# Kernel optimization log

Measured on AMD Instinct MI355X. Metric: run time of the kernel, lower is better.

## Reference

```python
import jax, jax.numpy as jnp
import numpy as np

N = 100_000        # nodes
F_IN = 1024        # input features
H1, C1 = 8, 8      # layer-1 heads, per-head channels (concat -> 64)
C_OUT = 40         # num classes (layer-2, heads=1, concat=False)
E = 3_200_000      # directed edges (avg degree 32)
NEG_SLOPE = 0.2    # PyG GATConv default leaky_relu slope


def setup_inputs() -> dict:
    key = jax.random.key(0)
    ks = jax.random.split(key, 10)
    x = jax.random.normal(ks[0], (N, F_IN), jnp.float32)
    edge_index = jax.random.randint(ks[1], (2, E), 0, N, dtype=jnp.int32)
    s1 = 1.0 / np.sqrt(F_IN)
    W1 = jax.random.normal(ks[2], (F_IN, H1 * C1), jnp.float32) * s1
    sa = 1.0 / np.sqrt(C1)
    att_src1 = jax.random.normal(ks[3], (H1, C1), jnp.float32) * sa
    att_dst1 = jax.random.normal(ks[4], (H1, C1), jnp.float32) * sa
    b1 = jnp.zeros((H1 * C1,), jnp.float32)
    s2 = 1.0 / np.sqrt(H1 * C1)
    W2 = jax.random.normal(ks[5], (H1 * C1, C_OUT), jnp.float32) * s2
    so = 1.0 / np.sqrt(C_OUT)
    att_src2 = jax.random.normal(ks[6], (1, C_OUT), jnp.float32) * so
    att_dst2 = jax.random.normal(ks[7], (1, C_OUT), jnp.float32) * so
    b2 = jnp.zeros((C_OUT,), jnp.float32)
    return {"x": x, "edge_index": edge_index, "W1": W1, "att_src1": att_src1,
            "att_dst1": att_dst1, "b1": b1, "W2": W2, "att_src2": att_src2,
            "att_dst2": att_dst2, "b2": b2}


def gat_layer(x, src, dst, W, a_src, a_dst, b, heads, ch, concat, n):
    # per-head linear projection: [n, heads, ch]
    xw = (x @ W).reshape(n, heads, ch)
    # per-node attention logits: [n, heads]
    al_src = jnp.einsum('nhc,hc->nh', xw, a_src)
    al_dst = jnp.einsum('nhc,hc->nh', xw, a_dst)
    # per-edge scores (message src -> dst): [e, heads]
    e = jax.nn.leaky_relu(al_src[src] + al_dst[dst], NEG_SLOPE)
    # segment softmax over incoming edges of each dst node
    m = jax.ops.segment_max(e, dst, num_segments=n)          # [n, heads]
    p = jnp.exp(e - m[dst])
    denom = jax.ops.segment_sum(p, dst, num_segments=n)      # [n, heads]
    alpha = p / (denom[dst] + 1e-16)                          # [e, heads]
    # weighted scatter-sum of source features
    out = jax.ops.segment_sum(xw[src] * alpha[:, :, None], dst, num_segments=n)
    out = out.reshape(n, heads * ch) if concat else out.mean(axis=1)
    return out + b


def reference(x, edge_index, W1, att_src1, att_dst1, b1, W2, att_src2, att_dst2, b2):
    n = x.shape[0]
    # PyG GATConv default: add self loops
    loop = jnp.arange(n, dtype=edge_index.dtype)
    src = jnp.concatenate([edge_index[0], loop])
    dst = jnp.concatenate([edge_index[1], loop])
    h = jax.nn.elu(gat_layer(x, src, dst, W1, att_src1, att_dst1, b1, H1, C1, True, n))
    h = gat_layer(h, src, dst, W2, att_src2, att_dst2, b2, 1, C_OUT, False, n)
    return jax.nn.log_softmax(h, axis=1)
```

## Files before the change

kernel.cpp:

```cpp
#include <hip/hip_runtime.h>
#include <hip/hip_bf16.h>
#include <cstdint>
#include <cstddef>

#define F_IN 1024
#define F1 64
#define H1 8
#define C1 8
#define C_OUT 40
#define XW2S 64
#define NEG 0.2f
#define LOG2E 1.442695040888963387f
#define B1 256
#define BSHIFT 9
#define BNODES 512

typedef __attribute__((ext_vector_type(8))) short short8;
typedef __attribute__((ext_vector_type(4))) float f32x4;

static __device__ __forceinline__ unsigned short f2bf(float f) {
  union { float f; unsigned u; } v; v.f = f;
  unsigned r = v.u + 0x7fff + ((v.u >> 16) & 1);
  return (unsigned short)(r >> 16);
}
static __device__ __forceinline__ float bf2f(unsigned short h) {
  union { unsigned u; float f; } v; v.u = ((unsigned)h) << 16; return v.f;
}
static __device__ __forceinline__ unsigned pkbf(float a, float b) {
  union { __hip_bfloat162 h; unsigned u; } c;
  c.h = __float22bfloat162_rn(float2{a, b});
  return c.u;
}
static __device__ __forceinline__ int rfl(int v) {
  return __builtin_amdgcn_readfirstlane(v);
}

__global__ __launch_bounds__(256) void w1cvt_kernel(const float* __restrict__ W1,
                                                    unsigned short* __restrict__ w1t) {
  int i = blockIdx.x * 256 + threadIdx.x;
  int c = i >> 10, k = i & 1023;
  w1t[i] = f2bf(W1[(size_t)k * F1 + c]);
}

__global__ __launch_bounds__(256) void gemm1_mfma(const float* __restrict__ x,
                                                  const unsigned short* __restrict__ w1t,
                                                  unsigned short* __restrict__ xw1, int n) {
  const int tid = threadIdx.x;
  const int wv = tid >> 6;
  const int l = tid & 63;
  const int lr = l & 15;
  const int lg = l >> 4;
  const int rowBase = blockIdx.x * 128 + wv * 32;
  int r0 = rowBase + lr, r1 = rowBase + 16 + lr;
  int r0c = r0 < n ? r0 : (n - 1);
  int r1c = r1 < n ? r1 : (n - 1);
  const float* px0 = x + (size_t)r0c * F_IN + lg * 8;
  const float* px1 = x + (size_t)r1c * F_IN + lg * 8;

  f32x4 acc00 = {0.f,0.f,0.f,0.f}, acc01 = acc00, acc02 = acc00, acc03 = acc00;
  f32x4 acc10 = acc00, acc11 = acc00, acc12 = acc00, acc13 = acc00;

#pragma unroll 2
  for (int k0 = 0; k0 < F_IN; k0 += 32) {
    float4 xa0 = *(const float4*)(px0 + k0);
    float4 xb0 = *(const float4*)(px0 + k0 + 4);
    float4 xa1 = *(const float4*)(px1 + k0);
    float4 xb1 = *(const float4*)(px1 + k0 + 4);
    union { short8 s; unsigned u[4]; } a0, a1;
    a0.u[0] = pkbf(xa0.x, xa0.y); a0.u[1] = pkbf(xa0.z, xa0.w);
    a0.u[2] = pkbf(xb0.x, xb0.y); a0.u[3] = pkbf(xb0.z, xb0.w);
    a1.u[0] = pkbf(xa1.x, xa1.y); a1.u[1] = pkbf(xa1.z, xa1.w);
    a1.u[2] = pkbf(xb1.x, xb1.y); a1.u[3] = pkbf(xb1.z, xb1.w);
    const size_t kOff = (size_t)(k0 + lg * 8);
    short8 b0 = *(const short8*)(w1t + (size_t)(0 * 16 + lr) * F_IN + kOff);
    short8 b1 = *(const short8*)(w1t + (size_t)(1 * 16 + lr) * F_IN + kOff);
    short8 b2 = *(const short8*)(w1t + (size_t)(2 * 16 + lr) * F_IN + kOff);
    short8 b3 = *(const short8*)(w1t + (size_t)(3 * 16 + lr) * F_IN + kOff);
    acc00 = __builtin_amdgcn_mfma_f32_16x16x32_bf16(a0.s, b0, acc00, 0, 0, 0);
    acc01 = __builtin_amdgcn_mfma_f32_16x16x32_bf16(a0.s, b1, acc01, 0, 0, 0);
    acc02 = __builtin_amdgcn_mfma_f32_16x16x32_bf16(a0.s, b2, acc02, 0, 0, 0);
    acc03 = __builtin_amdgcn_mfma_f32_16x16x32_bf16(a0.s, b3, acc03, 0, 0, 0);
    acc10 = __builtin_amdgcn_mfma_f32_16x16x32_bf16(a1.s, b0, acc10, 0, 0, 0);
    acc11 = __builtin_amdgcn_mfma_f32_16x16x32_bf16(a1.s, b1, acc11, 0, 0, 0);
    acc12 = __builtin_amdgcn_mfma_f32_16x16x32_bf16(a1.s, b2, acc12, 0, 0, 0);
    acc13 = __builtin_amdgcn_mfma_f32_16x16x32_bf16(a1.s, b3, acc13, 0, 0, 0);
  }

#pragma unroll
  for (int r = 0; r < 4; ++r) {
    int o0 = rowBase + lg * 4 + r;
    if (o0 < n) {
      unsigned short* po = xw1 + (size_t)o0 * F1 + lr;
      po[0]  = f2bf(acc00[r]);
      po[16] = f2bf(acc01[r]);
      po[32] = f2bf(acc02[r]);
      po[48] = f2bf(acc03[r]);
    }
    int o1 = rowBase + 16 + lg * 4 + r;
    if (o1 < n) {
      unsigned short* po = xw1 + (size_t)o1 * F1 + lr;
      po[0]  = f2bf(acc10[r]);
      po[16] = f2bf(acc11[r]);
      po[32] = f2bf(acc12[r]);
      po[48] = f2bf(acc13[r]);
    }
  }
}

__global__ __launch_bounds__(256) void al1_kernel(const unsigned short* __restrict__ xw1,
    const float* __restrict__ asrc, const float* __restrict__ adst,
    float* __restrict__ al_src, float* __restrict__ al_dst, int n) {
  int id = blockIdx.x * 256 + threadIdx.x;
  if (id >= n * H1) return;
  int node = id >> 3, h = id & 7;
  const unsigned short* row = xw1 + (size_t)node * F1 + h * C1;
  float s = 0.f, d = 0.f;
#pragma unroll
  for (int c = 0; c < C1; ++c) {
    float v = bf2f(row[c]);
    s += v * asrc[h * C1 + c];
    d += v * adst[h * C1 + c];
  }
  al_src[id] = s * LOG2E;
  al_dst[id] = d * LOG2E;
}

__global__ __launch_bounds__(256) void binhist_kernel(const int* __restrict__ dst,
    int* __restrict__ cnt, int e, int nbuck) {
  __shared__ int lh[256];
  int tid = threadIdx.x, blk = blockIdx.x;
  lh[tid] = 0;
  __syncthreads();
  int chunk = (e + gridDim.x - 1) / gridDim.x;
  int s = blk * chunk, en = min(e, s + chunk);
  for (int i = s + tid; i < en; i += 256) atomicAdd(&lh[dst[i] >> BSHIFT], 1);
  __syncthreads();
  if (tid < nbuck) cnt[tid * B1 + blk] = lh[tid];
}

__global__ __launch_bounds__(256) void scan1_kernel(const int* __restrict__ in,
    int* __restrict__ excl, int* __restrict__ bsum, int len) {
  __shared__ int s[256];
  int tid = threadIdx.x;
  int gid = blockIdx.x * 256 + tid;
  int v = gid < len ? in[gid] : 0;
  s[tid] = v;
  __syncthreads();
  for (int ofs = 1; ofs < 256; ofs <<= 1) {
    int t = (tid >= ofs) ? s[tid - ofs] : 0;
    __syncthreads();
    s[tid] += t;
    __syncthreads();
  }
  if (gid < len) excl[gid] = s[tid] - v;
  if (tid == 255) bsum[blockIdx.x] = s[255];
}

__global__ __launch_bounds__(1024) void scan2_kernel(int* __restrict__ bsum, int nb) {
  __shared__ int s[1024];
  int tid = threadIdx.x;
  int v = tid < nb ? bsum[tid] : 0;
  s[tid] = v;
  __syncthreads();
  for (int ofs = 1; ofs < 1024; ofs <<= 1) {
    int t = (tid >= ofs) ? s[tid - ofs] : 0;
    __syncthreads();
    s[tid] += t;
    __syncthreads();
  }
  if (tid < nb) bsum[tid] = s[tid] - v;
}

__global__ __launch_bounds__(256) void binscatter_kernel(const int* __restrict__ src,
    const int* __restrict__ dst, const int* __restrict__ cntS,
    const int* __restrict__ bsum, unsigned* __restrict__ binned, int e, int nbuck) {
  __shared__ int lcur[256];
  int tid = threadIdx.x, blk = blockIdx.x;
  if (tid < nbuck) lcur[tid] = cntS[tid * B1 + blk] + bsum[tid];
  __syncthreads();
  int chunk = (e + gridDim.x - 1) / gridDim.x;
  int s = blk * chunk, en = min(e, s + chunk);
  for (int i = s + tid; i < en; i += 256) {
    int d = dst[i];
    int pos = atomicAdd(&lcur[d >> BSHIFT], 1);
    binned[pos] = ((unsigned)(d & (BNODES - 1)) << 23) | (unsigned)src[i];
  }
}

__global__ __launch_bounds__(256) void bucket_csr_kernel(const unsigned* __restrict__ binned,
    const int* __restrict__ bsum, int* __restrict__ deg, int* __restrict__ off,
    int* __restrict__ csr, int e, int n, int nbuck) {
  int q = blockIdx.x, tid = threadIdx.x;
  int eBase = bsum[q];
  int eEnd = (q + 1 < nbuck) ? bsum[q + 1] : e;
  __shared__ int nh[BNODES], sc[BNODES], cu[BNODES];
  nh[tid] = 0; nh[tid + 256] = 0;
  __syncthreads();
  for (int i = eBase + tid; i < eEnd; i += 256) atomicAdd(&nh[binned[i] >> 23], 1);
  __syncthreads();
  sc[tid] = nh[tid]; sc[tid + 256] = nh[tid + 256];
  __syncthreads();
  for (int ofs = 1; ofs < BNODES; ofs <<= 1) {
    int a0 = sc[tid], a1 = sc[tid + 256];
    int b0 = (tid >= ofs) ? sc[tid - ofs] : 0;
    int b1 = (tid + 256 >= ofs) ? sc[tid + 256 - ofs] : 0;
    __syncthreads();
    sc[tid] = a0 + b0; sc[tid + 256] = a1 + b1;
    __syncthreads();
  }
  int e0 = sc[tid] - nh[tid], e1 = sc[tid + 256] - nh[tid + 256];
  cu[tid] = e0; cu[tid + 256] = e1;
  int node0 = q * BNODES + tid, node1 = node0 + 256;
  if (node0 < n) { deg[node0] = nh[tid];       off[node0] = eBase + e0; }
  if (node1 < n) { deg[node1] = nh[tid + 256]; off[node1] = eBase + e1; }
  __syncthreads();
  for (int i = eBase + tid; i < eEnd; i += 256) {
    unsigned v = binned[i];
    int pos = eBase + atomicAdd(&cu[v >> 23], 1);
    csr[pos] = (int)(v & 0x7FFFFF);
  }
}

__global__ __launch_bounds__(256) void gat1_agg(const unsigned short* __restrict__ xw1,
    const float* __restrict__ al_src, const float* __restrict__ al_dst,
    const int* __restrict__ csr, const int* __restrict__ off, const int* __restrict__ deg,
    const float* __restrict__ b1, float* __restrict__ h1, int n) {
  const int node = rfl((int)((blockIdx.x * blockDim.x + threadIdx.x) >> 6));
  if (node >= n) return;
  const int lane = threadIdx.x & 63;
  const int half = lane >> 5;
  const int c2 = lane & 31;
  const int h = c2 >> 2;
  const int base = rfl(off[node]);
  const int cnt = rfl(deg[node]);
  const float adst = al_dst[node * H1 + h];
  const int* __restrict__ csrp = csr + base;
  const char* xwB = (const char*)xw1;
  const char* alB = (const char*)al_src;
  const int cOff = c2 << 2;
  const int hOff = h << 2;

  float acc0 = 0.f, acc1 = 0.f, l = 0.f;

#define PAIR_BODY(wv_, av_) { \
    float t = (av_) + adst; \
    float sc = fmaxf(t, NEG * t); \
    float p = __builtin_amdgcn_exp2f(sc); \
    acc0 = fmaf(p, bf2f((unsigned short)((wv_) & 0xffffu)), acc0); \
    acc1 = fmaf(p, bf2f((unsigned short)((wv_) >> 16)), acc1); \
    l += p; }

  int it = 0;
  for (; it + 8 <= cnt; it += 8) {
    int xo[4];
#pragma unroll
    for (int jp = 0; jp < 4; ++jp) {
      int s0 = rfl(csrp[it + 2 * jp]) << 7;
      int s1 = rfl(csrp[it + 2 * jp + 1]) << 7;
      xo[jp] = half ? s1 : s0;
    }
    unsigned wv[4]; float av[4];
#pragma unroll
    for (int jp = 0; jp < 4; ++jp) {
      wv[jp] = *(const unsigned*)(xwB + xo[jp] + cOff);
      av[jp] = *(const float*)(alB + (xo[jp] >> 2) + hOff);
    }
#pragma unroll
    for (int jp = 0; jp < 4; ++jp) PAIR_BODY(wv[jp], av[jp]);
  }
  for (; it + 2 <= cnt; it += 2) {
    int s0 = rfl(csrp[it]) << 7;
    int s1 = rfl(csrp[it + 1]) << 7;
    int bs = half ? s1 : s0;
    unsigned w = *(const unsigned*)(xwB + bs + cOff);
    float av = *(const float*)(alB + (bs >> 2) + hOff);
    PAIR_BODY(w, av);
  }
  {
    const bool odd = (it < cnt);
    int sA = odd ? rfl(csrp[it]) : node;
    int bs = (half ? node : sA) << 7;
    unsigned w = *(const unsigned*)(xwB + bs + cOff);
    float av = *(const float*)(alB + (bs >> 2) + hOff);
    float t = av + adst;
    float sc = fmaxf(t, NEG * t);
    float p = __builtin_amdgcn_exp2f(sc);
    if (!odd && half) p = 0.f;
    acc0 = fmaf(p, bf2f((unsigned short)(w & 0xffffu)), acc0);
    acc1 = fmaf(p, bf2f((unsigned short)(w >> 16)), acc1);
    l += p;
  }
#undef PAIR_BODY

  acc0 += __shfl_xor(acc0, 32);
  acc1 += __shfl_xor(acc1, 32);
  l    += __shfl_xor(l, 32);
  if (half == 0) {
    float inv = 1.f / (l + 1e-16f);
    float2 bv = *(const float2*)(b1 + (c2 << 1));
    float o0 = acc0 * inv + bv.x;
    float o1 = acc1 * inv + bv.y;
    o0 = o0 > 0.f ? o0 : __expf(o0) - 1.f;
    o1 = o1 > 0.f ? o1 : __expf(o1) - 1.f;
    *(float2*)(h1 + (size_t)node * F1 + (c2 << 1)) = make_float2(o0, o1);
  }
}

__global__ __launch_bounds__(256) void gemm2_kernel(const float* __restrict__ h1,
    const float* __restrict__ W2, const float* __restrict__ asrc,
    const float* __restrict__ adst, unsigned short* __restrict__ xw2,
    float* __restrict__ alS2, float* __restrict__ alD2, int n) {
  __shared__ float ws[F1 * C_OUT];
  __shared__ float wsa[C_OUT], wsd[C_OUT];
  int tid = threadIdx.x;
  for (int i = tid; i < F1 * C_OUT; i += 256) ws[i] = W2[i];
  if (tid < C_OUT) { wsa[tid] = asrc[tid]; wsd[tid] = adst[tid]; }
  __syncthreads();
  int node = blockIdx.x * 256 + tid;
  if (node >= n) return;
  const float4* row4 = (const float4*)(h1 + (size_t)node * F1);
  float acc[C_OUT];
#pragma unroll
  for (int j = 0; j < C_OUT; ++j) acc[j] = 0.f;
#pragma unroll 2
  for (int k4 = 0; k4 < 16; ++k4) {
    float4 xv = row4[k4];
    const float* w0 = &ws[(4 * k4 + 0) * C_OUT];
    const float* w1 = &ws[(4 * k4 + 1) * C_OUT];
    const float* w2 = &ws[(4 * k4 + 2) * C_OUT];
    const float* w3 = &ws[(4 * k4 + 3) * C_OUT];
#pragma unroll
    for (int j = 0; j < C_OUT; j += 4) {
      float4 v0 = *(const float4*)(w0 + j);
      float4 v1 = *(const float4*)(w1 + j);
      float4 v2 = *(const float4*)(w2 + j);
      float4 v3 = *(const float4*)(w3 + j);
      acc[j + 0] += xv.x * v0.x + xv.y * v1.x + xv.z * v2.x + xv.w * v3.x;
      acc[j + 1] += xv.x * v0.y + xv.y * v1.y + xv.z * v2.y + xv.w * v3.y;
      acc[j + 2] += xv.x * v0.z + xv.y * v1.z + xv.z * v2.z + xv.w * v3.z;
      acc[j + 3] += xv.x * v0.w + xv.y * v1.w + xv.z * v2.w + xv.w * v3.w;
    }
  }
  float s = 0.f, d = 0.f;
#pragma unroll
  for (int j = 0; j < C_OUT; ++j) { s += acc[j] * wsa[j]; d += acc[j] * wsd[j]; }
  alS2[node] = s * LOG2E;
  alD2[node] = d * LOG2E;
  unsigned short* orow = xw2 + (size_t)node * XW2S;
#pragma unroll
  for (int j = 0; j < C_OUT; j += 4) {
    ushort4 o;
    o.x = f2bf(acc[j + 0]); o.y = f2bf(acc[j + 1]);
    o.z = f2bf(acc[j + 2]); o.w = f2bf(acc[j + 3]);
    *(ushort4*)(orow + j) = o;
  }
}

__global__ __launch_bounds__(256) void gat2_agg(const unsigned short* __restrict__ xw2,
    const float* __restrict__ alS, const float* __restrict__ alD,
    const int* __restrict__ csr, const int* __restrict__ off, const int* __restrict__ deg,
    const float* __restrict__ b2, float* __restrict__ out, int n) {
  const int node = rfl((int)((blockIdx.x * blockDim.x + threadIdx.x) >> 6));
  if (node >= n) return;
  const int lane = threadIdx.x & 63;
  const int half = lane >> 5;
  const int c2 = lane & 31;
  const bool act = c2 < 20;
  const int c2r = act ? c2 : 0;
  const int base = rfl(off[node]);
  const int cnt = rfl(deg[node]);
  const float adst = alD[node];
  const int* __restrict__ csrp = csr + base;
  const char* xwB = (const char*)xw2;
  const char* alB = (const char*)alS;
  const int cOff = c2r << 2;

  float acc0 = 0.f, acc1 = 0.f, l = 0.f;

#define PAIR_BODY2(wv_, av_) { \
    float t = (av_) + adst; \
    float sc = fmaxf(t, NEG * t); \
    float p = __builtin_amdgcn_exp2f(sc); \
    acc0 = fmaf(p, bf2f((unsigned short)((wv_) & 0xffffu)), acc0); \
    acc1 = fmaf(p, bf2f((unsigned short)((wv_) >> 16)), acc1); \
    l += p; }

  int it = 0;
  for (; it + 8 <= cnt; it += 8) {
    int xo[4];
#pragma unroll
    for (int jp = 0; jp < 4; ++jp) {
      int s0 = rfl(csrp[it + 2 * jp]) << 7;
      int s1 = rfl(csrp[it + 2 * jp + 1]) << 7;
      xo[jp] = half ? s1 : s0;
    }
    unsigned wv[4]; float av[4];
#pragma unroll
    for (int jp = 0; jp < 4; ++jp) {
      wv[jp] = *(const unsigned*)(xwB + xo[jp] + cOff);
      av[jp] = *(const float*)(alB + (xo[jp] >> 5));
    }
#pragma unroll
    for (int jp = 0; jp < 4; ++jp) PAIR_BODY2(wv[jp], av[jp]);
  }
  for (; it + 2 <= cnt; it += 2) {
    int s0 = rfl(csrp[it]) << 7;
    int s1 = rfl(csrp[it + 1]) << 7;
    int bs = half ? s1 : s0;
    unsigned w = *(const unsigned*)(xwB + bs + cOff);
    float av = *(const float*)(alB + (bs >> 5));
    PAIR_BODY2(w, av);
  }
  {
    const bool odd = (it < cnt);
    int sA = odd ? rfl(csrp[it]) : node;
    int bs = (half ? node : sA) << 7;
    unsigned w = *(const unsigned*)(xwB + bs + cOff);
    float av = *(const float*)(alB + (bs >> 5));
    float t = av + adst;
    float sc = fmaxf(t, NEG * t);
    float p = __builtin_amdgcn_exp2f(sc);
    if (!odd && half) p = 0.f;
    acc0 = fmaf(p, bf2f((unsigned short)(w & 0xffffu)), acc0);
    acc1 = fmaf(p, bf2f((unsigned short)(w >> 16)), acc1);
    l += p;
  }
#undef PAIR_BODY2

  acc0 += __shfl_xor(acc0, 32);
  acc1 += __shfl_xor(acc1, 32);
  l    += __shfl_xor(l, 32);

  float inv = 1.f / (l + 1e-16f);
  float v0 = -1e30f, v1 = -1e30f;
  if (act) {
    float2 bv = *(const float2*)(b2 + (c2 << 1));
    v0 = acc0 * inv + bv.x;
    v1 = acc1 * inv + bv.y;
  }
  float mx = fmaxf(v0, v1);
#pragma unroll
  for (int mask = 1; mask <= 16; mask <<= 1) mx = fmaxf(mx, __shfl_xor(mx, mask));
  float e0 = act ? __expf(v0 - mx) : 0.f;
  float e1 = act ? __expf(v1 - mx) : 0.f;
  float sum = e0 + e1;
#pragma unroll
  for (int mask = 1; mask <= 16; mask <<= 1) sum += __shfl_xor(sum, mask);
  if (half == 0 && act) {
    float ls = __logf(sum);
    *(float2*)(out + (size_t)node * C_OUT + (c2 << 1)) =
        make_float2(v0 - mx - ls, v1 - mx - ls);
  }
}

extern "C" void kernel_launch(void* const* d_in, const int* in_sizes, int n_in,
                              void* d_out, int out_size, void* d_ws, size_t ws_size,
                              hipStream_t stream) {
  const float* x   = (const float*)d_in[0];
  const int*   ei  = (const int*)d_in[1];
  const float* W1  = (const float*)d_in[2];
  const float* as1 = (const float*)d_in[3];
  const float* ad1 = (const float*)d_in[4];
  const float* b1  = (const float*)d_in[5];
  const float* W2  = (const float*)d_in[6];
  const float* as2 = (const float*)d_in[7];
  const float* ad2 = (const float*)d_in[8];
  const float* b2  = (const float*)d_in[9];
  float* out = (float*)d_out;

  const int n = in_sizes[0] / F_IN;
  const int e = in_sizes[1] / 2;
  const int* srcIdx = ei;
  const int* dstIdx = ei + e;
  const int nbuck = (n + BNODES - 1) >> BSHIFT;
  const int clen = nbuck * B1;

  char* p = (char*)d_ws;
  auto take = [&](size_t bytes) {
    char* q = p;
    p += (bytes + 255) & ~(size_t)255;
    return q;
  };
  unsigned short* xw1 = (unsigned short*)take((size_t)n * F1 * 2);
  float* h1           = (float*)take((size_t)n * F1 * 4);
  unsigned short* xw2 = (unsigned short*)take((size_t)n * XW2S * 2);
  unsigned short* w1t = (unsigned short*)take((size_t)F_IN * F1 * 2);
  float* alS1 = (float*)take((size_t)n * H1 * 4);
  float* alD1 = (float*)take((size_t)n * H1 * 4);
  float* alS2 = (float*)take((size_t)n * 4);
  float* alD2 = (float*)take((size_t)n * 4);
  int* deg  = (int*)take((size_t)n * 4);
  int* offb = (int*)take((size_t)n * 4);
  int* cnt  = (int*)take((size_t)clen * 4);
  int* cntS = (int*)take((size_t)clen * 4);
  int* bsum = (int*)take(4096);
  unsigned* binned = (unsigned*)take((size_t)e * 4);
  int* csr  = (int*)take((size_t)e * 4);

  dim3 b256(256);
  w1cvt_kernel<<<dim3((F_IN * F1) / 256), b256, 0, stream>>>(W1, w1t);
  gemm1_mfma<<<dim3((n + 127) / 128), b256, 0, stream>>>(x, w1t, xw1, n);
  al1_kernel<<<dim3((n * H1 + 255) / 256), b256, 0, stream>>>(xw1, as1, ad1, alS1, alD1, n);

  binhist_kernel<<<dim3(B1), b256, 0, stream>>>(dstIdx, cnt, e, nbuck);
  int nbScan = (clen + 255) / 256;
  scan1_kernel<<<dim3(nbScan), b256, 0, stream>>>(cnt, cntS, bsum, clen);
  scan2_kernel<<<dim3(1), dim3(1024), 0, stream>>>(bsum, nbScan);
  binscatter_kernel<<<dim3(B1), b256, 0, stream>>>(srcIdx, dstIdx, cntS, bsum, binned, e, nbuck);
  bucket_csr_kernel<<<dim3(nbuck), b256, 0, stream>>>(binned, bsum, deg, offb, csr, e, n, nbuck);

  gat1_agg<<<dim3((n + 3) / 4), b256, 0, stream>>>(xw1, alS1, alD1, csr, offb, deg, b1, h1, n);
  gemm2_kernel<<<dim3((n + 255) / 256), b256, 0, stream>>>(h1, W2, as2, ad2, xw2, alS2, alD2, n);
  gat2_agg<<<dim3((n + 3) / 4), b256, 0, stream>>>(xw2, alS2, alD2, csr, offb, deg, b2, out, n);
}
```

Before: 440.8 us.

## Fuse dst histogram into GEMM1 launch, enlarge GEMM tile, halve bucket size

The destination-bucket histogram now runs as extra blocks inside the first GEMM launch, so it overlaps with the x projection instead of running as its own kernel. The GEMM tile grows to 64 rows per wave (256 per block), reusing each W1 fragment load across four row groups. Buckets shrink to 256 nodes, giving more, smaller blocks for CSR construction and a simpler one-element-per-thread scan. Risks include fewer GEMM blocks to hide memory latency and higher register pressure.

```diff
diff --git a/kernel.cpp b/kernel.cpp
--- a/kernel.cpp
+++ b/kernel.cpp
@@ -12,8 +12,8 @@
 #define NEG 0.2f
 #define LOG2E 1.442695040888963387f
 #define B1 256
-#define BSHIFT 9
-#define BNODES 512
+#define BSHIFT 8
+#define BNODES 256
 
 typedef __attribute__((ext_vector_type(8))) short short8;
 typedef __attribute__((ext_vector_type(4))) float f32x4;
@@ -42,67 +42,89 @@
   w1t[i] = f2bf(W1[(size_t)k * F1 + c]);
 }
 
-__global__ __launch_bounds__(256) void gemm1_mfma(const float* __restrict__ x,
-                                                  const unsigned short* __restrict__ w1t,
-                                                  unsigned short* __restrict__ xw1, int n) {
+__global__ __launch_bounds__(256) void k1_hist_gemm(const float* __restrict__ x,
+    const unsigned short* __restrict__ w1t, unsigned short* __restrict__ xw1,
+    const int* __restrict__ dst, int* __restrict__ cnt, int n, int e, int nbuck) {
+  const int bid = blockIdx.x;
   const int tid = threadIdx.x;
+  if (bid < B1) {
+    __shared__ int lh[512];
+    lh[tid] = 0; lh[tid + 256] = 0;
+    __syncthreads();
+    int chunk = (e + B1 - 1) / B1;
+    int s = bid * chunk, en = min(e, s + chunk);
+    for (int i = s + tid; i < en; i += 256) atomicAdd(&lh[dst[i] >> BSHIFT], 1);
+    __syncthreads();
+    for (int b = tid; b < nbuck; b += 256) cnt[b * B1 + bid] = lh[b];
+    return;
+  }
+  const int gb = bid - B1;
   const int wv = tid >> 6;
   const int l = tid & 63;
   const int lr = l & 15;
   const int lg = l >> 4;
-  const int rowBase = blockIdx.x * 128 + wv * 32;
-  int r0 = rowBase + lr, r1 = rowBase + 16 + lr;
-  int r0c = r0 < n ? r0 : (n - 1);
-  int r1c = r1 < n ? r1 : (n - 1);
-  const float* px0 = x + (size_t)r0c * F_IN + lg * 8;
-  const float* px1 = x + (size_t)r1c * F_IN + lg * 8;
-
-  f32x4 acc00 = {0.f,0.f,0.f,0.f}, acc01 = acc00, acc02 = acc00, acc03 = acc00;
-  f32x4 acc10 = acc00, acc11 = acc00, acc12 = acc00, acc13 = acc00;
+  const int rowBase = gb * 256 + wv * 64;
+  const float* px0;
+  const float* px1;
+  const float* px2;
+  const float* px3;
+  {
+    int r0 = rowBase + 0 * 16 + lr;  px0 = x + (size_t)(r0 < n ? r0 : n - 1) * F_IN + lg * 8;
+    int r1 = rowBase + 1 * 16 + lr;  px1 = x + (size_t)(r1 < n ? r1 : n - 1) * F_IN + lg * 8;
+    int r2 = rowBase + 2 * 16 + lr;  px2 = x + (size_t)(r2 < n ? r2 : n - 1) * F_IN + lg * 8;
+    int r3 = rowBase + 3 * 16 + lr;  px3 = x + (size_t)(r3 < n ? r3 : n - 1) * F_IN + lg * 8;
+  }
+
+  f32x4 acc[4][4];
+#pragma unroll
+  for (int s = 0; s < 4; ++s)
+#pragma unroll
+    for (int j = 0; j < 4; ++j) acc[s][j] = (f32x4){0.f, 0.f, 0.f, 0.f};
 
 #pragma unroll 2
   for (int k0 = 0; k0 < F_IN; k0 += 32) {
-    float4 xa0 = *(const float4*)(px0 + k0);
-    float4 xb0 = *(const float4*)(px0 + k0 + 4);
-    float4 xa1 = *(const float4*)(px1 + k0);
-    float4 xb1 = *(const float4*)(px1 + k0 + 4);
-    union { short8 s; unsigned u[4]; } a0, a1;
-    a0.u[0] = pkbf(xa0.x, xa0.y); a0.u[1] = pkbf(xa0.z, xa0.w);
-    a0.u[2] = pkbf(xb0.x, xb0.y); a0.u[3] = pkbf(xb0.z, xb0.w);
-    a1.u[0] = pkbf(xa1.x, xa1.y); a1.u[1] = pkbf(xa1.z, xa1.w);
-    a1.u[2] = pkbf(xb1.x, xb1.y); a1.u[3] = pkbf(xb1.z, xb1.w);
+    union { short8 s; unsigned u[4]; } a[4];
+    {
+      float4 xa, xb;
+      xa = *(const float4*)(px0 + k0); xb = *(const float4*)(px0 + k0 + 4);
+      a[0].u[0] = pkbf(xa.x, xa.y); a[0].u[1] = pkbf(xa.z, xa.w);
+      a[0].u[2] = pkbf(xb.x, xb.y); a[0].u[3] = pkbf(xb.z, xb.w);
+      xa = *(const float4*)(px1 + k0); xb = *(const float4*)(px1 + k0 + 4);
+      a[1].u[0] = pkbf(xa.x, xa.y); a[1].u[1] = pkbf(xa.z, xa.w);
+      a[1].u[2] = pkbf(xb.x, xb.y); a[1].u[3] = pkbf(xb.z, xb.w);
+      xa = *(const float4*)(px2 + k0); xb = *(const float4*)(px2 + k0 + 4);
+      a[2].u[0] = pkbf(xa.x, xa.y); a[2].u[1] = pkbf(xa.z, xa.w);
+      a[2].u[2] = pkbf(xb.x, xb.y); a[2].u[3] = pkbf(xb.z, xb.w);
+      xa = *(const float4*)(px3 + k0); xb = *(const float4*)(px3 + k0 + 4);
+      a[3].u[0] = pkbf(xa.x, xa.y); a[3].u[1] = pkbf(xa.z, xa.w);
+      a[3].u[2] = pkbf(xb.x, xb.y); a[3].u[3] = pkbf(xb.z, xb.w);
+    }
     const size_t kOff = (size_t)(k0 + lg * 8);
     short8 b0 = *(const short8*)(w1t + (size_t)(0 * 16 + lr) * F_IN + kOff);
     short8 b1 = *(const short8*)(w1t + (size_t)(1 * 16 + lr) * F_IN + kOff);
     short8 b2 = *(const short8*)(w1t + (size_t)(2 * 16 + lr) * F_IN + kOff);
     short8 b3 = *(const short8*)(w1t + (size_t)(3 * 16 + lr) * F_IN + kOff);
-    acc00 = __builtin_amdgcn_mfma_f32_16x16x32_bf16(a0.s, b0, acc00, 0, 0, 0);
-    acc01 = __builtin_amdgcn_mfma_f32_16x16x32_bf16(a0.s, b1, acc01, 0, 0, 0);
-    acc02 = __builtin_amdgcn_mfma_f32_16x16x32_bf16(a0.s, b2, acc02, 0, 0, 0);
-    acc03 = __builtin_amdgcn_mfma_f32_16x16x32_bf16(a0.s, b3, acc03, 0, 0, 0);
-    acc10 = __builtin_amdgcn_mfma_f32_16x16x32_bf16(a1.s, b0, acc10, 0, 0, 0);
-    acc11 = __builtin_amdgcn_mfma_f32_16x16x32_bf16(a1.s, b1, acc11, 0, 0, 0);
-    acc12 = __builtin_amdgcn_mfma_f32_16x16x32_bf16(a1.s, b2, acc12, 0, 0, 0);
-    acc13 = __builtin_amdgcn_mfma_f32_16x16x32_bf16(a1.s, b3, acc13, 0, 0, 0);
-  }
-
-#pragma unroll
-  for (int r = 0; r < 4; ++r) {
-    int o0 = rowBase + lg * 4 + r;
-    if (o0 < n) {
-      unsigned short* po = xw1 + (size_t)o0 * F1 + lr;
-      po[0]  = f2bf(acc00[r]);
-      po[16] = f2bf(acc01[r]);
-      po[32] = f2bf(acc02[r]);
-      po[48] = f2bf(acc03[r]);
-    }
-    int o1 = rowBase + 16 + lg * 4 + r;
-    if (o1 < n) {
-      unsigned short* po = xw1 + (size_t)o1 * F1 + lr;
-      po[0]  = f2bf(acc10[r]);
-      po[16] = f2bf(acc11[r]);
-      po[32] = f2bf(acc12[r]);
-      po[48] = f2bf(acc13[r]);
+#pragma unroll
+    for (int s = 0; s < 4; ++s) {
+      acc[s][0] = __builtin_amdgcn_mfma_f32_16x16x32_bf16(a[s].s, b0, acc[s][0], 0, 0, 0);
+      acc[s][1] = __builtin_amdgcn_mfma_f32_16x16x32_bf16(a[s].s, b1, acc[s][1], 0, 0, 0);
+      acc[s][2] = __builtin_amdgcn_mfma_f32_16x16x32_bf16(a[s].s, b2, acc[s][2], 0, 0, 0);
+      acc[s][3] = __builtin_amdgcn_mfma_f32_16x16x32_bf16(a[s].s, b3, acc[s][3], 0, 0, 0);
+    }
+  }
+
+#pragma unroll
+  for (int s = 0; s < 4; ++s) {
+#pragma unroll
+    for (int r = 0; r < 4; ++r) {
+      int orow = rowBase + s * 16 + lg * 4 + r;
+      if (orow < n) {
+        unsigned short* po = xw1 + (size_t)orow * F1 + lr;
+        po[0]  = f2bf(acc[s][0][r]);
+        po[16] = f2bf(acc[s][1][r]);
+        po[32] = f2bf(acc[s][2][r]);
+        po[48] = f2bf(acc[s][3][r]);
+      }
     }
   }
 }
@@ -125,19 +147,6 @@
   al_dst[id] = d * LOG2E;
 }
 
-__global__ __launch_bounds__(256) void binhist_kernel(const int* __restrict__ dst,
-    int* __restrict__ cnt, int e, int nbuck) {
-  __shared__ int lh[256];
-  int tid = threadIdx.x, blk = blockIdx.x;
-  lh[tid] = 0;
-  __syncthreads();
-  int chunk = (e + gridDim.x - 1) / gridDim.x;
-  int s = blk * chunk, en = min(e, s + chunk);
-  for (int i = s + tid; i < en; i += 256) atomicAdd(&lh[dst[i] >> BSHIFT], 1);
-  __syncthreads();
-  if (tid < nbuck) cnt[tid * B1 + blk] = lh[tid];
-}
-
 __global__ __launch_bounds__(256) void scan1_kernel(const int* __restrict__ in,
     int* __restrict__ excl, int* __restrict__ bsum, int len) {
   __shared__ int s[256];
@@ -174,9 +183,9 @@
 __global__ __launch_bounds__(256) void binscatter_kernel(const int* __restrict__ src,
     const int* __restrict__ dst, const int* __restrict__ cntS,
     const int* __restrict__ bsum, unsigned* __restrict__ binned, int e, int nbuck) {
-  __shared__ int lcur[256];
+  __shared__ int lcur[512];
   int tid = threadIdx.x, blk = blockIdx.x;
-  if (tid < nbuck) lcur[tid] = cntS[tid * B1 + blk] + bsum[tid];
+  for (int b = tid; b < nbuck; b += 256) lcur[b] = cntS[b * B1 + blk] + bsum[b];
   __syncthreads();
   int chunk = (e + gridDim.x - 1) / gridDim.x;
   int s = blk * chunk, en = min(e, s + chunk);
@@ -194,30 +203,28 @@
   int eBase = bsum[q];
   int eEnd = (q + 1 < nbuck) ? bsum[q + 1] : e;
   __shared__ int nh[BNODES], sc[BNODES], cu[BNODES];
-  nh[tid] = 0; nh[tid + 256] = 0;
+  nh[tid] = 0;
   __syncthreads();
   for (int i = eBase + tid; i < eEnd; i += 256) atomicAdd(&nh[binned[i] >> 23], 1);
   __syncthreads();
-  sc[tid] = nh[tid]; sc[tid + 256] = nh[tid + 256];
+  int v = nh[tid];
+  sc[tid] = v;
   __syncthreads();
   for (int ofs = 1; ofs < BNODES; ofs <<= 1) {
-    int a0 = sc[tid], a1 = sc[tid + 256];
-    int b0 = (tid >= ofs) ? sc[tid - ofs] : 0;
-    int b1 = (tid + 256 >= ofs) ? sc[tid + 256 - ofs] : 0;
-    __syncthreads();
-    sc[tid] = a0 + b0; sc[tid + 256] = a1 + b1;
-    __syncthreads();
-  }
-  int e0 = sc[tid] - nh[tid], e1 = sc[tid + 256] - nh[tid + 256];
-  cu[tid] = e0; cu[tid + 256] = e1;
-  int node0 = q * BNODES + tid, node1 = node0 + 256;
-  if (node0 < n) { deg[node0] = nh[tid];       off[node0] = eBase + e0; }
-  if (node1 < n) { deg[node1] = nh[tid + 256]; off[node1] = eBase + e1; }
+    int t = (tid >= ofs) ? sc[tid - ofs] : 0;
+    __syncthreads();
+    sc[tid] += t;
+    __syncthreads();
+  }
+  int ex = sc[tid] - v;
+  cu[tid] = ex;
+  int node0 = q * BNODES + tid;
+  if (node0 < n) { deg[node0] = v; off[node0] = eBase + ex; }
   __syncthreads();
   for (int i = eBase + tid; i < eEnd; i += 256) {
-    unsigned v = binned[i];
-    int pos = eBase + atomicAdd(&cu[v >> 23], 1);
-    csr[pos] = (int)(v & 0x7FFFFF);
+    unsigned w = binned[i];
+    int pos = eBase + atomicAdd(&cu[w >> 23], 1);
+    csr[pos] = (int)(w & 0x7FFFFF);
   }
 }
 
@@ -498,11 +505,11 @@
   int* csr  = (int*)take((size_t)e * 4);
 
   dim3 b256(256);
+  const int gB = (n + 255) / 256;
   w1cvt_kernel<<<dim3((F_IN * F1) / 256), b256, 0, stream>>>(W1, w1t);
-  gemm1_mfma<<<dim3((n + 127) / 128), b256, 0, stream>>>(x, w1t, xw1, n);
+  k1_hist_gemm<<<dim3(B1 + gB), b256, 0, stream>>>(x, w1t, xw1, dstIdx, cnt, n, e, nbuck);
   al1_kernel<<<dim3((n * H1 + 255) / 256), b256, 0, stream>>>(xw1, as1, ad1, alS1, alD1, n);
 
-  binhist_kernel<<<dim3(B1), b256, 0, stream>>>(dstIdx, cnt, e, nbuck);
   int nbScan = (clen + 255) / 256;
   scan1_kernel<<<dim3(nbScan), b256, 0, stream>>>(cnt, cntS, bsum, clen);
   scan2_kernel<<<dim3(1), dim3(1024), 0, stream>>>(bsum, nbScan);
```

Result: no change. 440.8 us (-0.0%).
